# Optimization experiments

Measured on AMD Instinct MI355X. Metric: run time of the kernel, lower is better.

## Reference

```python
import jax, jax.numpy as jnp
import numpy as np

NC = 80
REG_MAX = 16          # detect head reg_max; BboxLoss uses REG_MAX-1 = 15
TOPK = 10
ALPHA = 0.5
BETA = 6.0
EPS = 1e-9
HYP_BOX, HYP_CLS, HYP_DFL = 7.5, 0.5, 1.5


def _make_anchors():
    # 640x640 image, strides 8/16/32 -> grids 80/40/20; offset 0.5 (grid units)
    pts, strd = [], []
    for hw, s in ((80, 8.0), (40, 16.0), (20, 32.0)):
        sx = np.arange(hw, dtype=np.float32) + 0.5
        sy, sxg = np.meshgrid(sx, sx, indexing='ij')
        pts.append(np.stack([sxg, sy], -1).reshape(-1, 2))
        strd.append(np.full((hw * hw, 1), s, np.float32))
    return np.concatenate(pts), np.concatenate(strd)


def ciou(box1, box2, eps=1e-7):
    """CIoU, mirrors torch compute_iou (eps added to heights only)."""
    b1x1, b1y1, b1x2, b1y2 = jnp.split(box1, 4, -1)
    b2x1, b2y1, b2x2, b2y2 = jnp.split(box2, 4, -1)
    w1, h1 = b1x2 - b1x1, b1y2 - b1y1 + eps
    w2, h2 = b2x2 - b2x1, b2y2 - b2y1 + eps
    inter = (jnp.clip(jnp.minimum(b1x2, b2x2) - jnp.maximum(b1x1, b2x1), 0)
             * jnp.clip(jnp.minimum(b1y2, b2y2) - jnp.maximum(b1y1, b2y1), 0))
    union = w1 * h1 + w2 * h2 - inter + eps
    iou = inter / union
    cw = jnp.maximum(b1x2, b2x2) - jnp.minimum(b1x1, b2x1)
    ch = jnp.maximum(b1y2, b2y2) - jnp.minimum(b1y1, b2y1)
    c2 = cw ** 2 + ch ** 2 + eps
    rho2 = ((b2x1 + b2x2 - b1x1 - b1x2) ** 2 + (b2y1 + b2y2 - b1y1 - b1y2) ** 2) / 4
    v = (4.0 / np.pi ** 2) * (jnp.arctan(w2 / h2) - jnp.arctan(w1 / h1)) ** 2
    alpha = jax.lax.stop_gradient(v / (v - iou + (1 + eps)))  # torch: with no_grad
    return iou - (rho2 / c2 + v * alpha)


def _assigner(ps, pb, anc, gt_labels, gt_bboxes, mask_gt):
    """TaskAlignedAssigner. ps:[B,A,NC] sigmoid scores, pb:[B,A,4] pixel boxes,
    anc:[A,2] pixel anchor points. Returns (target_bboxes, target_scores, fg_mask)."""
    B, A, _ = ps.shape
    M = gt_bboxes.shape[1]
    lt, rb = gt_bboxes[..., :2], gt_bboxes[..., 2:]                      # [B,M,2]
    deltas = jnp.concatenate([anc[None, None] - lt[:, :, None],
                              rb[:, :, None] - anc[None, None]], -1)     # [B,M,A,4]
    mask_in = deltas.min(-1) > EPS                                       # [B,M,A]
    mgt = mask_in & (mask_gt[:, :, None] > 0)                            # bool [B,M,A]
    mgtf = mgt.astype(ps.dtype)
    # bbox_scores[b,m,a] = ps[b,a,gt_labels[b,m]] where mgt else 0
    bsc = ps[jnp.arange(B)[:, None], :, gt_labels]                       # [B,M,A]
    bbox_scores = jnp.where(mgt, bsc, 0.0)
    ov = jnp.clip(ciou(gt_bboxes[:, :, None], pb[:, None])[..., 0], 0)   # [B,M,A]
    overlaps = jnp.where(mgt, ov, 0.0)
    align = bbox_scores ** ALPHA * overlaps ** BETA
    tkm, tki = jax.lax.top_k(align, TOPK)                                # [B,M,K]
    keep = (tkm > EPS) & jnp.take_along_axis(mgt, tki, -1)
    tki = jnp.where(keep, tki, 0)                                        # masked -> 0 (as torch)
    bidx = jnp.arange(B)[:, None, None]
    midx = jnp.arange(M)[None, :, None]
    cnt = jnp.zeros((B, M, A), jnp.int32).at[bidx, midx, tki].add(1)
    mask_topk = jnp.minimum(cnt, 1).astype(ps.dtype)
    mask_pos = mask_topk * mgtf                                          # [B,M,A]
    fg = mask_pos.sum(-2)                                                # [B,A]
    # resolve anchors assigned to multiple GTs by max overlap (no-op if none)
    multi = fg[:, None, :] > 1
    max_idx = overlaps.argmax(1)                                         # [B,A]
    is_max = (jnp.arange(M)[None, :, None] == max_idx[:, None, :]).astype(mask_pos.dtype)
    mask_pos = jnp.where(multi, is_max, mask_pos)
    fg = mask_pos.sum(-2)
    tgt_idx = mask_pos.argmax(-2)                                        # [B,A]
    tlab = jnp.clip(jnp.take_along_axis(gt_labels, tgt_idx, 1), 0)       # [B,A]
    tbox = jnp.take_along_axis(gt_bboxes, tgt_idx[..., None], 1)         # [B,A,4]
    tscores = jax.nn.one_hot(tlab, NC, dtype=ps.dtype) * (fg[..., None] > 0)
    align = align * mask_pos
    pos_align = align.max(-1, keepdims=True)                             # [B,M,1]
    pos_ov = (overlaps * mask_pos).max(-1, keepdims=True)
    norm = (align * pos_ov / (pos_align + EPS)).max(-2)[..., None]       # [B,A,1]
    return tbox, tscores * norm, fg > 0


def _loss(pred_scores, pred_distri, anchor_points, stride_tensor, gt_bboxes, mask_gt, gt_labels):
    B, A, _ = pred_scores.shape
    # box decode (DFL expectation)
    proj = jnp.arange(REG_MAX, dtype=pred_distri.dtype)
    dist = jax.nn.softmax(pred_distri.reshape(B, A, 4, REG_MAX), -1) @ proj  # [B,A,4]
    lt, rb = dist[..., :2], dist[..., 2:]
    pred_bboxes = jnp.concatenate([anchor_points - lt, anchor_points + rb], -1)  # grid units
    sg = jax.lax.stop_gradient  # assigner is @torch.no_grad
    tbox, tscores, fg = _assigner(sg(jax.nn.sigmoid(pred_scores)),
                                  sg(pred_bboxes * stride_tensor),
                                  anchor_points * stride_tensor,
                                  gt_labels, gt_bboxes, mask_gt)
    tss = jnp.maximum(tscores.sum(), 1.0)
    # BCEWithLogits, sum / tss
    x = pred_scores
    bce = jnp.maximum(x, 0) - x * tscores + jnp.log1p(jnp.exp(-jnp.abs(x)))
    loss_cls = bce.sum() / tss
    # bbox + DFL losses (masked reductions instead of masked_select)
    tbox = tbox / stride_tensor
    weight = tscores.sum(-1)                                             # [B,A]
    fgf = fg.astype(weight.dtype)
    iou = ciou(pred_bboxes, tbox)[..., 0]                                # [B,A]
    loss_iou = ((1.0 - iou) * weight * fgf).sum() / tss
    rm = REG_MAX - 1                                                     # BboxLoss reg_max = 15
    tgt = jnp.clip(jnp.concatenate([anchor_points - tbox[..., :2],
                                    tbox[..., 2:] - anchor_points], -1), 0, rm - 0.01)  # [B,A,4]
    logp = jax.nn.log_softmax(pred_distri.reshape(B, A, 4, REG_MAX), -1)
    tl = tgt.astype(jnp.int32)
    wl = (tl + 1).astype(tgt.dtype) - tgt
    wr = 1.0 - wl
    left = -jnp.take_along_axis(logp, tl[..., None], -1)[..., 0]
    right = -jnp.take_along_axis(logp, (tl + 1)[..., None], -1)[..., 0]
    dfl = (left * wl + right * wr).mean(-1)                              # [B,A]
    loss_dfl = (dfl * weight * fgf).sum() / tss
    return jnp.stack([loss_iou * HYP_BOX, loss_cls * HYP_CLS, loss_dfl * HYP_DFL])


def setup_inputs() -> dict:
    key = jax.random.key(0)
    k0, k1, k2, k3, k4, k5 = jax.random.split(key, 6)
    B, A, M = 32, 8400, 40
    pred_scores = jax.random.normal(k0, (B, A, NC), jnp.float32)
    pred_distri = jax.random.normal(k1, (B, A, 4 * REG_MAX), jnp.float32)
    anc, strd = _make_anchors()
    cxy = jax.random.uniform(k2, (B, M, 2)) * 640.0
    wh = jax.random.uniform(k3, (B, M, 2)) * 150.0 + 10.0
    gt_bboxes = jnp.concatenate([jnp.clip(cxy - wh / 2, 0, 640),
                                 jnp.clip(cxy + wh / 2, 0, 640)], -1)
    mask_gt = (jax.random.uniform(k4, (B, M)) < 0.8).astype(jnp.float32)
    gt_labels = jax.random.randint(k5, (B, M), 0, NC)
    return {"pred_scores": pred_scores, "pred_distri": pred_distri,
            "anchor_points": jnp.asarray(anc), "stride_tensor": jnp.asarray(strd),
            "gt_bboxes": gt_bboxes, "mask_gt": mask_gt, "gt_labels": gt_labels}


def reference(pred_scores, pred_distri, anchor_points, stride_tensor, gt_bboxes, mask_gt, gt_labels):
    return _loss(pred_scores, pred_distri, anchor_points, stride_tensor, gt_bboxes, mask_gt, gt_labels)
```

## Files before the change

kernel.cpp:

```cpp
#include <hip/hip_runtime.h>
#include <math.h>

#define B_    32
#define A_    8400
#define M_    40
#define NC_   80
#define TOPK_ 10
#define EPS_  1e-9f

__device__ __forceinline__ float ciou_f(float b1x1, float b1y1, float b1x2, float b1y2,
                                        float b2x1, float b2y1, float b2x2, float b2y2) {
    const float eps = 1e-7f;
    float w1 = b1x2 - b1x1, h1 = b1y2 - b1y1 + eps;
    float w2 = b2x2 - b2x1, h2 = b2y2 - b2y1 + eps;
    float iw = fminf(b1x2, b2x2) - fmaxf(b1x1, b2x1);
    float ih = fminf(b1y2, b2y2) - fmaxf(b1y1, b2y1);
    float inter = fmaxf(iw, 0.f) * fmaxf(ih, 0.f);
    float uni = w1 * h1 + w2 * h2 - inter + eps;
    float iou = inter / uni;
    float cw = fmaxf(b1x2, b2x2) - fminf(b1x1, b2x1);
    float ch = fmaxf(b1y2, b2y2) - fminf(b1y1, b2y1);
    float c2 = cw * cw + ch * ch + eps;
    float dx = b2x1 + b2x2 - b1x1 - b1x2;
    float dy = b2y1 + b2y2 - b1y1 - b1y2;
    float rho2 = (dx * dx + dy * dy) * 0.25f;
    float da = atanf(w2 / h2) - atanf(w1 / h1);
    float v = 0.4052847345693511f * da * da;
    float alpha = v / (v - iou + 1.f + eps);
    return iou - (rho2 / c2 + v * alpha);
}

__device__ __forceinline__ void anchor_of(int a, float& ax, float& ay, float& s) {
    if (a < 6400)      { s = 8.f;  int r = a;        ax = (float)(r % 80) + 0.5f; ay = (float)(r / 80) + 0.5f; }
    else if (a < 8000) { s = 16.f; int r = a - 6400; ax = (float)(r % 40) + 0.5f; ay = (float)(r / 40) + 0.5f; }
    else               { s = 32.f; int r = a - 8000; ax = (float)(r % 20) + 0.5f; ay = (float)(r / 20) + 0.5f; }
}

__device__ __forceinline__ float ov_at2(const float* __restrict__ pb,
                                        float g0, float g1, float g2, float g3,
                                        int b, int a) {
    float ax, ay, s; anchor_of(a, ax, ay, s);
    float axp = ax * s, ayp = ay * s;
    if (!((axp - g0) > EPS_ && (ayp - g1) > EPS_ && (g2 - axp) > EPS_ && (g3 - ayp) > EPS_))
        return 0.f;
    const float4 p = *(const float4*)(pb + ((size_t)b * A_ + a) * 4);
    float c = ciou_f(g0, g1, g2, g3, p.x * s, p.y * s, p.z * s, p.w * s);
    return fmaxf(c, 0.f);
}

__device__ __forceinline__ unsigned long long shflxor_u64(unsigned long long v, int m) {
    int lo = __shfl_xor((int)(unsigned)(v & 0xffffffffull), m, 64);
    int hi = __shfl_xor((int)(unsigned)(v >> 32), m, 64);
    return ((unsigned long long)(unsigned)hi << 32) | (unsigned)lo;
}

__device__ __forceinline__ void dfl_quad(float4 v, int f, float* __restrict__ pb) {
    int q = f & 3;
    float e0 = __expf(v.x), e1 = __expf(v.y), e2 = __expf(v.z), e3 = __expf(v.w);
    float se = e0 + e1 + e2 + e3;
    float sd = e1 + 2.f * e2 + 3.f * e3 + (float)(4 * q) * se;
    se += __shfl_xor(se, 1, 64); se += __shfl_xor(se, 2, 64);
    sd += __shfl_xor(sd, 1, 64); sd += __shfl_xor(sd, 2, 64);
    float dist = sd / se;
    float d1 = __shfl_down(dist, 4, 64);
    float d2 = __shfl_down(dist, 8, 64);
    float d3 = __shfl_down(dist, 12, 64);
    if ((f & 15) == 0) {
        int aidx = f >> 4;
        int a = aidx % A_;
        float ax, ay, s; anchor_of(a, ax, ay, s);
        ((float4*)pb)[aidx] = make_float4(ax - dist, ay - d1, ax + d2, ay + d3);
    }
}

__device__ __forceinline__ float bce4(float4 x) {
    return fmaxf(x.x, 0.f) + __logf(1.f + __expf(-fabsf(x.x)))
         + fmaxf(x.y, 0.f) + __logf(1.f + __expf(-fabsf(x.y)))
         + fmaxf(x.z, 0.f) + __logf(1.f + __expf(-fabsf(x.z)))
         + fmaxf(x.w, 0.f) + __logf(1.f + __expf(-fabsf(x.w)));
}

__global__ void k_stream(const float4* __restrict__ d4,
                         const float4* __restrict__ s4,
                         float* __restrict__ pb,
                         unsigned long long* __restrict__ abits64,
                         unsigned long long* __restrict__ ovmax,
                         float* __restrict__ acc) {
    const int tid0 = blockIdx.x * blockDim.x + threadIdx.x;
    const int nthr = gridDim.x * blockDim.x;
    for (int i = tid0; i < B_ * A_; i += nthr) {
        abits64[i] = 0ull;
        ovmax[i] = 0x00000000FFFFFFFFull;
    }
    const int NF4 = B_ * A_ * 16;
    for (int base = tid0; base < NF4; base += 4 * nthr) {
        int f1 = base + nthr, f2 = base + 2 * nthr, f3 = base + 3 * nthr;
        float4 v0 = d4[base];
        float4 v1, v2, v3;
        if (f1 < NF4) v1 = d4[f1];
        if (f2 < NF4) v2 = d4[f2];
        if (f3 < NF4) v3 = d4[f3];
        dfl_quad(v0, base, pb);
        if (f1 < NF4) dfl_quad(v1, f1, pb);
        if (f2 < NF4) dfl_quad(v2, f2, pb);
        if (f3 < NF4) dfl_quad(v3, f3, pb);
    }
    const int N4 = B_ * A_ * (NC_ / 4);
    float sum = 0.f;
    for (int base = tid0; base < N4; base += 4 * nthr) {
        int f1 = base + nthr, f2 = base + 2 * nthr, f3 = base + 3 * nthr;
        float4 x0 = s4[base];
        float4 x1, x2, x3;
        if (f1 < N4) x1 = s4[f1];
        if (f2 < N4) x2 = s4[f2];
        if (f3 < N4) x3 = s4[f3];
        sum += bce4(x0);
        if (f1 < N4) sum += bce4(x1);
        if (f2 < N4) sum += bce4(x2);
        if (f3 < N4) sum += bce4(x3);
    }
    __shared__ float sh[256];
    sh[threadIdx.x] = sum; __syncthreads();
    for (int s = 128; s > 0; s >>= 1) {
        if (threadIdx.x < s) sh[threadIdx.x] += sh[threadIdx.x + s];
        __syncthreads();
    }
    if (threadIdx.x == 0) atomicAdd(&acc[1], sh[0]);
}

__global__ __launch_bounds__(64) void k_aligntopk(
    const float* __restrict__ scores, const float* __restrict__ pb,
    const float* __restrict__ gt, const float* __restrict__ mgt,
    const int* __restrict__ glab, unsigned int* __restrict__ abits,
    unsigned long long* __restrict__ ovmax) {
    int bm = blockIdx.x;
    if (mgt[bm] <= 0.f) return;
    int b = bm / M_, m = bm % M_;
    int lab = glab[bm];
    const float g0 = gt[bm * 4 + 0], g1 = gt[bm * 4 + 1];
    const float g2 = gt[bm * 4 + 2], g3 = gt[bm * 4 + 3];
    int lane = threadIdx.x;

    const int   Wl[3]  = { 80, 40, 20 };
    const int   Bs[3]  = { 0, 6400, 8000 };
    const float Sl[3]  = { 8.f, 16.f, 32.f };
    int jlo[3], ilo[3], rw[3], cnt[3];
#pragma unroll
    for (int l = 0; l < 3; l++) {
        float s = Sl[l]; int W = Wl[l];
        int jl = max(0, (int)floorf(g0 / s - 0.5f) - 1);
        int jh = min(W - 1, (int)ceilf(g2 / s - 0.5f) + 1);
        int il = max(0, (int)floorf(g1 / s - 0.5f) - 1);
        int ih = min(W - 1, (int)ceilf(g3 / s - 0.5f) + 1);
        int w = jh - jl + 1, h = ih - il + 1;
        jlo[l] = jl; ilo[l] = il; rw[l] = max(w, 0);
        cnt[l] = (w > 0 && h > 0) ? w * h : 0;
    }
    int c01 = cnt[0] + cnt[1];
    int tot = c01 + cnt[2];

    unsigned long long t[TOPK_];
#pragma unroll
    for (int k = 0; k < TOPK_; k++) t[k] = 0ull;

    for (int c = lane; c < tot; c += 64) {
        int l = (c < cnt[0]) ? 0 : ((c < c01) ? 1 : 2);
        int r = c - ((l == 0) ? 0 : ((l == 1) ? cnt[0] : c01));
        int w = rw[l];
        int di = r / w, dj = r - di * w;
        int i = ilo[l] + di, j = jlo[l] + dj;
        float s = Sl[l];
        float ax = ((float)j + 0.5f) * s;
        float ay = ((float)i + 0.5f) * s;
        if (!((ax - g0) > EPS_ && (ay - g1) > EPS_ && (g2 - ax) > EPS_ && (g3 - ay) > EPS_))
            continue;
        int a = Bs[l] + i * Wl[l] + j;
        const float4 p = *(const float4*)(pb + ((size_t)b * A_ + a) * 4);
        float ci = ciou_f(g0, g1, g2, g3, p.x * s, p.y * s, p.z * s, p.w * s);
        float ov = fmaxf(ci, 0.f);
        float al = 0.f;
        if (ov > 0.f) {
            unsigned long long opk = ((unsigned long long)__float_as_uint(ov) << 32)
                                     | (unsigned)(~(unsigned)m);
            atomicMax(&ovmax[(size_t)b * A_ + a], opk);
            float sc = scores[((size_t)b * A_ + a) * NC_ + lab];
            float bs = 1.f / (1.f + __expf(-sc));
            float o2 = ov * ov;
            al = sqrtf(bs) * o2 * o2 * o2;
        }
        unsigned long long pkd = ((unsigned long long)__float_as_uint(al) << 32)
                                 | (unsigned)(~(unsigned)a);
        if (pkd > t[TOPK_ - 1]) {
            unsigned long long cv = pkd;
#pragma unroll
            for (int k = 0; k < TOPK_; k++) {
                bool g = cv > t[k];
                unsigned long long o = t[k];
                t[k] = g ? cv : o;
                cv   = g ? o : cv;
            }
        }
    }

    unsigned long long mysel = 0ull;
#pragma unroll
    for (int k = 0; k < TOPK_; k++) {
        unsigned long long w = t[0];
#pragma unroll
        for (int off = 32; off >= 1; off >>= 1) {
            unsigned long long o = shflxor_u64(w, off);
            if (o > w) w = o;
        }
        if (lane == k) mysel = w;
        if (w != 0ull && t[0] == w) {
#pragma unroll
            for (int q = 0; q < TOPK_ - 1; q++) t[q] = t[q + 1];
            t[TOPK_ - 1] = 0ull;
        }
    }

    float sval = __uint_as_float((unsigned)(mysel >> 32));
    int   sidx = (int)(~(unsigned)mysel);
    unsigned int bit = 1u << (m & 31);
    int word = (m >= 32) ? 1 : 0;
    bool keep = (lane < TOPK_) && (sval > EPS_);
    if (keep) atomicOr(&abits[2 * ((size_t)b * A_ + sidx) + word], bit);
    unsigned long long kb = __ballot(keep);
    if (lane == 0 && __popcll(kb) < TOPK_) {
        float ax = 4.f, ay = 4.f;
        if ((ax - g0) > EPS_ && (ay - g1) > EPS_ && (g2 - ax) > EPS_ && (g3 - ay) > EPS_)
            atomicOr(&abits[2 * ((size_t)b * A_) + word], bit);
    }
}

__global__ __launch_bounds__(256) void k_R(
    const unsigned int* __restrict__ abits,
    const unsigned long long* __restrict__ ovmax,
    const float* __restrict__ pb,
    const float* __restrict__ scores, const float* __restrict__ gt,
    const int* __restrict__ glab,
    int* __restrict__ tgti, float* __restrict__ alv,
    int* __restrict__ pa_g, int* __restrict__ po_g) {
    int idx = blockIdx.x * blockDim.x + threadIdx.x;
    if (idx >= B_ * A_) return;
    unsigned int lo = abits[2 * idx], hi = abits[2 * idx + 1];
    int fg = __popc(lo) + __popc(hi);
    if (fg == 0) { tgti[idx] = -1; return; }
    int b = idx / A_, a = idx % A_;
    int tgt; float ov;
    if (fg > 1) {
        unsigned long long pk = ovmax[idx];
        tgt = (int)(~(unsigned)(pk & 0xffffffffull));
        ov  = __uint_as_float((unsigned)(pk >> 32));
    } else {
        tgt = lo ? (__ffs(lo) - 1) : (32 + __ffs(hi) - 1);
        int bmi = b * M_ + tgt;
        ov = ov_at2(pb, gt[bmi * 4], gt[bmi * 4 + 1], gt[bmi * 4 + 2], gt[bmi * 4 + 3], b, a);
    }
    float al = 0.f;
    if (ov > 0.f) {
        int lab = glab[b * M_ + tgt];
        float sc = scores[(size_t)idx * NC_ + lab];
        float bs = 1.f / (1.f + __expf(-sc));
        float o2 = ov * ov;
        al = sqrtf(bs) * o2 * o2 * o2;
    }
    tgti[idx] = tgt;
    alv[idx] = al;
    int bmi = b * M_ + tgt;
    atomicMax(&pa_g[bmi], __float_as_int(al));
    atomicMax(&po_g[bmi], __float_as_int(ov));
}

__global__ __launch_bounds__(256) void k_S(
    const int* __restrict__ tgti, const float* __restrict__ alv,
    const int* __restrict__ pa_g, const int* __restrict__ po_g,
    const float* __restrict__ scores, const float* __restrict__ pb,
    const float* __restrict__ gt, const int* __restrict__ glab,
    const float* __restrict__ distri, float* __restrict__ acc) {
    int idx = blockIdx.x * blockDim.x + threadIdx.x;
    float ts = 0.f, cs = 0.f, liou = 0.f, ldfl = 0.f;
    if (idx < B_ * A_) {
        int tgt = tgti[idx];
        if (tgt >= 0) {
            int b = idx / A_, a = idx % A_;
            int bmi = b * M_ + tgt;
            float al = alv[idx];
            float pa = __int_as_float(pa_g[bmi]);
            float po = __int_as_float(po_g[bmi]);
            float nv = al * po / (pa + EPS_);
            ts = nv;
            int lab = max(glab[bmi], 0);
            float sc = scores[(size_t)idx * NC_ + lab];
            cs = -sc * nv;
            float ax, ay, s; anchor_of(a, ax, ay, s);
            const float* g = gt + (size_t)bmi * 4;
            float t0 = g[0] / s, t1 = g[1] / s, t2 = g[2] / s, t3 = g[3] / s;
            const float4 p = *(const float4*)(pb + (size_t)idx * 4);
            float iou = ciou_f(p.x, p.y, p.z, p.w, t0, t1, t2, t3);
            liou = (1.f - iou) * nv;
            float tg[4] = { ax - t0, ay - t1, t2 - ax, t3 - ay };
            const float* dd = distri + (size_t)idx * 64;
            float dfl = 0.f;
#pragma unroll
            for (int sd = 0; sd < 4; sd++) {
                float tvv = fminf(fmaxf(tg[sd], 0.f), 14.99f);
                int tl = (int)tvv;
                float wl = (float)(tl + 1) - tvv;
                float wr = 1.f - wl;
                const float* xx = dd + sd * 16;
                float mx = xx[0];
#pragma unroll
                for (int j = 1; j < 16; j++) mx = fmaxf(mx, xx[j]);
                float se = 0.f;
#pragma unroll
                for (int j = 0; j < 16; j++) se += __expf(xx[j] - mx);
                float lse = mx + __logf(se);
                dfl += (lse - xx[tl]) * wl + (lse - xx[tl + 1]) * wr;
            }
            ldfl = dfl * 0.25f * nv;
        }
    }
    __shared__ float r0[256], r1[256], r2[256], r3[256];
    int tid = threadIdx.x;
    r0[tid] = ts; r1[tid] = cs; r2[tid] = liou; r3[tid] = ldfl;
    __syncthreads();
    for (int s = 128; s > 0; s >>= 1) {
        if (tid < s) {
            r0[tid] += r0[tid + s]; r1[tid] += r1[tid + s];
            r2[tid] += r2[tid + s]; r3[tid] += r3[tid + s];
        }
        __syncthreads();
    }
    if (tid == 0) {
        atomicAdd(&acc[0], r0[0]); atomicAdd(&acc[1], r1[0]);
        atomicAdd(&acc[2], r2[0]); atomicAdd(&acc[3], r3[0]);
    }
}

__global__ void k_final(const float* __restrict__ acc, float* __restrict__ out) {
    if (threadIdx.x == 0) {
        float tss = fmaxf(acc[0], 1.f);
        out[0] = acc[2] / tss * 7.5f;
        out[1] = acc[1] / tss * 0.5f;
        out[2] = acc[3] / tss * 1.5f;
    }
}

extern "C" void kernel_launch(void* const* d_in, const int* in_sizes, int n_in,
                              void* d_out, int out_size, void* d_ws, size_t ws_size,
                              hipStream_t stream) {
    const float* scores = (const float*)d_in[0];
    const float* distri = (const float*)d_in[1];
    const float* gtb    = (const float*)d_in[4];
    const float* mgt    = (const float*)d_in[5];
    const int*   glab   = (const int*)d_in[6];
    float* out = (float*)d_out;

    unsigned long long* ovmax = (unsigned long long*)d_ws;
    float* pb    = (float*)(ovmax + (size_t)B_ * A_);
    float* alv   = pb + (size_t)B_ * A_ * 4;
    int*   tgti  = (int*)(alv + (size_t)B_ * A_);
    float* acc   = (float*)(tgti + (size_t)B_ * A_);
    int*   pa_g  = (int*)(acc + 4);
    int*   po_g  = pa_g + B_ * M_;
    unsigned int* abits = (unsigned int*)(po_g + B_ * M_);

    size_t zero_bytes = (4 + 2 * B_ * M_) * sizeof(int);
    hipMemsetAsync(acc, 0, zero_bytes, stream);

    k_stream<<<2048, 256, 0, stream>>>((const float4*)distri, (const float4*)scores, pb,
                                       (unsigned long long*)abits, ovmax, acc);
    k_aligntopk<<<B_ * M_, 64, 0, stream>>>(scores, pb, gtb, mgt, glab, abits, ovmax);
    k_R<<<1050, 256, 0, stream>>>(abits, ovmax, pb, scores, gtb, glab, tgti, alv, pa_g, po_g);
    k_S<<<1050, 256, 0, stream>>>(tgti, alv, pa_g, po_g, scores, pb, gtb, glab, distri, acc);
    k_final<<<1, 64, 0, stream>>>(acc, out);
    (void)in_sizes; (void)n_in; (void)out_size; (void)ws_size;
}
```

Baseline: 285.7 us.

## Use DPP lane ops, fixed-trip unrolled streaming loads, and hoist score load

Swaps the shuffle-based quad reductions and shifts in the DFL decode for DPP row operations, and rebuilds the wave-wide u64 max in the top-k selection from DPP, swizzle and a single shuffle. The streaming kernel now assumes a fixed total thread count (NTHR) and issues 8-11 independent float4 loads per thread with no loop, aiming for more memory-level parallelism. The class-score load in the align kernel moves ahead of the CIoU math so its latency overlaps with compute, at the cost of loading it even for zero-overlap anchors. The hard-coded NTHR ties correctness to the launch grid size.

```diff
diff --git a/kernel.cpp b/kernel.cpp
--- a/kernel.cpp
+++ b/kernel.cpp
@@ -7,6 +7,8 @@
 #define NC_   80
 #define TOPK_ 10
 #define EPS_  1e-9f
+
+#define NTHR  524288
 
 __device__ __forceinline__ float ciou_f(float b1x1, float b1y1, float b1x2, float b1y2,
                                         float b2x1, float b2y1, float b2x2, float b2y2) {
@@ -54,17 +56,52 @@
     return ((unsigned long long)(unsigned)hi << 32) | (unsigned)lo;
 }
 
+__device__ __forceinline__ float qsum_dpp(float v) {
+    int y = __builtin_amdgcn_update_dpp(0, __float_as_int(v), 0xB1, 0xF, 0xF, true);
+    float r = v + __int_as_float(y);
+    int z = __builtin_amdgcn_update_dpp(0, __float_as_int(r), 0x4E, 0xF, 0xF, true);
+    return r + __int_as_float(z);
+}
+
+template <int CTRL>
+__device__ __forceinline__ unsigned long long dpp64(unsigned long long v) {
+    unsigned lo = (unsigned)__builtin_amdgcn_update_dpp(0, (int)(unsigned)v, CTRL, 0xF, 0xF, true);
+    unsigned hi = (unsigned)__builtin_amdgcn_update_dpp(0, (int)(unsigned)(v >> 32), CTRL, 0xF, 0xF, true);
+    return ((unsigned long long)hi << 32) | lo;
+}
+
+__device__ __forceinline__ unsigned long long max64(unsigned long long a, unsigned long long b) {
+    return a > b ? a : b;
+}
+
+__device__ __forceinline__ unsigned long long swz16_64(unsigned long long v) {
+    unsigned lo = (unsigned)__builtin_amdgcn_ds_swizzle((int)(unsigned)v, 0x401F);
+    unsigned hi = (unsigned)__builtin_amdgcn_ds_swizzle((int)(unsigned)(v >> 32), 0x401F);
+    return ((unsigned long long)hi << 32) | lo;
+}
+
+__device__ __forceinline__ unsigned long long wave_max_u64(unsigned long long w) {
+    w = max64(w, dpp64<0xB1>(w));
+    w = max64(w, dpp64<0x4E>(w));
+    w = max64(w, dpp64<0x141>(w));
+    w = max64(w, dpp64<0x140>(w));
+    w = max64(w, swz16_64(w));
+    w = max64(w, shflxor_u64(w, 32));
+    return w;
+}
+
 __device__ __forceinline__ void dfl_quad(float4 v, int f, float* __restrict__ pb) {
     int q = f & 3;
     float e0 = __expf(v.x), e1 = __expf(v.y), e2 = __expf(v.z), e3 = __expf(v.w);
     float se = e0 + e1 + e2 + e3;
     float sd = e1 + 2.f * e2 + 3.f * e3 + (float)(4 * q) * se;
-    se += __shfl_xor(se, 1, 64); se += __shfl_xor(se, 2, 64);
-    sd += __shfl_xor(sd, 1, 64); sd += __shfl_xor(sd, 2, 64);
+    se = qsum_dpp(se);
+    sd = qsum_dpp(sd);
     float dist = sd / se;
-    float d1 = __shfl_down(dist, 4, 64);
-    float d2 = __shfl_down(dist, 8, 64);
-    float d3 = __shfl_down(dist, 12, 64);
+    int di = __float_as_int(dist);
+    float d1 = __int_as_float(__builtin_amdgcn_update_dpp(0, di, 0x104, 0xF, 0xF, true));
+    float d2 = __int_as_float(__builtin_amdgcn_update_dpp(0, di, 0x108, 0xF, 0xF, true));
+    float d3 = __int_as_float(__builtin_amdgcn_update_dpp(0, di, 0x10C, 0xF, 0xF, true));
     if ((f & 15) == 0) {
         int aidx = f >> 4;
         int a = aidx % A_;
@@ -87,37 +124,49 @@
                          unsigned long long* __restrict__ ovmax,
                          float* __restrict__ acc) {
     const int tid0 = blockIdx.x * blockDim.x + threadIdx.x;
-    const int nthr = gridDim.x * blockDim.x;
-    for (int i = tid0; i < B_ * A_; i += nthr) {
-        abits64[i] = 0ull;
-        ovmax[i] = 0x00000000FFFFFFFFull;
-    }
-    const int NF4 = B_ * A_ * 16;
-    for (int base = tid0; base < NF4; base += 4 * nthr) {
-        int f1 = base + nthr, f2 = base + 2 * nthr, f3 = base + 3 * nthr;
-        float4 v0 = d4[base];
-        float4 v1, v2, v3;
-        if (f1 < NF4) v1 = d4[f1];
-        if (f2 < NF4) v2 = d4[f2];
-        if (f3 < NF4) v3 = d4[f3];
-        dfl_quad(v0, base, pb);
-        if (f1 < NF4) dfl_quad(v1, f1, pb);
-        if (f2 < NF4) dfl_quad(v2, f2, pb);
-        if (f3 < NF4) dfl_quad(v3, f3, pb);
-    }
-    const int N4 = B_ * A_ * (NC_ / 4);
+    if (tid0 < B_ * A_) {
+        abits64[tid0] = 0ull;
+        ovmax[tid0] = 0x00000000FFFFFFFFull;
+    }
+    {
+        const int NF4 = B_ * A_ * 16;
+        float4 v0 = d4[tid0];
+        float4 v1 = d4[tid0 + NTHR];
+        float4 v2 = d4[tid0 + 2 * NTHR];
+        float4 v3 = d4[tid0 + 3 * NTHR];
+        float4 v4 = d4[tid0 + 4 * NTHR];
+        float4 v5 = d4[tid0 + 5 * NTHR];
+        float4 v6 = d4[tid0 + 6 * NTHR];
+        float4 v7 = d4[tid0 + 7 * NTHR];
+        dfl_quad(v0, tid0, pb);
+        dfl_quad(v1, tid0 + NTHR, pb);
+        dfl_quad(v2, tid0 + 2 * NTHR, pb);
+        dfl_quad(v3, tid0 + 3 * NTHR, pb);
+        dfl_quad(v4, tid0 + 4 * NTHR, pb);
+        dfl_quad(v5, tid0 + 5 * NTHR, pb);
+        dfl_quad(v6, tid0 + 6 * NTHR, pb);
+        dfl_quad(v7, tid0 + 7 * NTHR, pb);
+        int f8 = tid0 + 8 * NTHR;
+        if (f8 < NF4) dfl_quad(d4[f8], f8, pb);
+    }
     float sum = 0.f;
-    for (int base = tid0; base < N4; base += 4 * nthr) {
-        int f1 = base + nthr, f2 = base + 2 * nthr, f3 = base + 3 * nthr;
-        float4 x0 = s4[base];
-        float4 x1, x2, x3;
-        if (f1 < N4) x1 = s4[f1];
-        if (f2 < N4) x2 = s4[f2];
-        if (f3 < N4) x3 = s4[f3];
-        sum += bce4(x0);
-        if (f1 < N4) sum += bce4(x1);
-        if (f2 < N4) sum += bce4(x2);
-        if (f3 < N4) sum += bce4(x3);
+    {
+        const int N4 = B_ * A_ * (NC_ / 4);
+        float4 x0 = s4[tid0];
+        float4 x1 = s4[tid0 + NTHR];
+        float4 x2 = s4[tid0 + 2 * NTHR];
+        float4 x3 = s4[tid0 + 3 * NTHR];
+        float4 x4 = s4[tid0 + 4 * NTHR];
+        float4 x5 = s4[tid0 + 5 * NTHR];
+        float4 x6 = s4[tid0 + 6 * NTHR];
+        float4 x7 = s4[tid0 + 7 * NTHR];
+        sum += bce4(x0); sum += bce4(x1); sum += bce4(x2); sum += bce4(x3);
+        sum += bce4(x4); sum += bce4(x5); sum += bce4(x6); sum += bce4(x7);
+        float4 x8 = s4[tid0 + 8 * NTHR];
+        float4 x9 = s4[tid0 + 9 * NTHR];
+        sum += bce4(x8); sum += bce4(x9);
+        int f10 = tid0 + 10 * NTHR;
+        if (f10 < N4) sum += bce4(s4[f10]);
     }
     __shared__ float sh[256];
     sh[threadIdx.x] = sum; __syncthreads();
@@ -176,6 +225,7 @@
             continue;
         int a = Bs[l] + i * Wl[l] + j;
         const float4 p = *(const float4*)(pb + ((size_t)b * A_ + a) * 4);
+        float sc = scores[((size_t)b * A_ + a) * NC_ + lab];
         float ci = ciou_f(g0, g1, g2, g3, p.x * s, p.y * s, p.z * s, p.w * s);
         float ov = fmaxf(ci, 0.f);
         float al = 0.f;
@@ -183,7 +233,6 @@
             unsigned long long opk = ((unsigned long long)__float_as_uint(ov) << 32)
                                      | (unsigned)(~(unsigned)m);
             atomicMax(&ovmax[(size_t)b * A_ + a], opk);
-            float sc = scores[((size_t)b * A_ + a) * NC_ + lab];
             float bs = 1.f / (1.f + __expf(-sc));
             float o2 = ov * ov;
             al = sqrtf(bs) * o2 * o2 * o2;
@@ -205,12 +254,7 @@
     unsigned long long mysel = 0ull;
 #pragma unroll
     for (int k = 0; k < TOPK_; k++) {
-        unsigned long long w = t[0];
-#pragma unroll
-        for (int off = 32; off >= 1; off >>= 1) {
-            unsigned long long o = shflxor_u64(w, off);
-            if (o > w) w = o;
-        }
+        unsigned long long w = wave_max_u64(t[0]);
         if (lane == k) mysel = w;
         if (w != 0ull && t[0] == w) {
 #pragma unroll
```

Result: no change. 284.0 us (-0.6%).
